# Kernel tuning notes

Hardware: AMD Instinct MI355X
Metric: run time of the kernel (lower is better)

## Reference

```python
import jax, jax.numpy as jnp
import numpy as np
from jax import lax

FILTERS = [(1, 32), (2, 32), (3, 64), (4, 128), (5, 256), (6, 512), (7, 1024)]
CHAR_VOCAB, CHAR_DIM, MAX_CHARS = 262, 16, 50
N_FILTERS = sum(n for _, n in FILTERS)  # 2048
PROJ_DIM = 512
B, S = 16, 256


def setup_inputs() -> dict:
    key = jax.random.key(0)
    ks = jax.random.split(key, 32)
    inp = {}
    inp["words"] = jax.random.randint(ks[0], (B, S), 0, 50000)
    inp["chars"] = jax.random.randint(ks[1], (B, S, MAX_CHARS), 0, CHAR_VOCAB)
    inp["char_emb"] = jax.random.normal(ks[2], (CHAR_VOCAB, CHAR_DIM), jnp.float32) * 0.1
    for i, (w, n) in enumerate(FILTERS):
        inp[f"conv_w_{i}"] = jax.random.normal(ks[3 + i], (n, CHAR_DIM, w), jnp.float32) * 0.1
        inp[f"conv_b_{i}"] = jnp.zeros((n,), jnp.float32)
    for j in range(2):
        inp[f"hw_w_{j}"] = jax.random.normal(ks[12 + j], (2 * N_FILTERS, N_FILTERS), jnp.float32) * 0.02
        # Highway init: transform bias = 0, gate bias = 1
        inp[f"hw_b_{j}"] = jnp.concatenate([jnp.zeros((N_FILTERS,), jnp.float32), jnp.ones((N_FILTERS,), jnp.float32)])
    inp["proj_w"] = jax.random.normal(ks[20], (PROJ_DIM, N_FILTERS), jnp.float32) * 0.02
    inp["proj_b"] = jnp.zeros((PROJ_DIM,), jnp.float32)
    return inp


def _char_cnn(chars, char_emb, conv_ws, conv_bs, hw_ws, hw_bs, proj_w, proj_b):
    b, s, L = chars.shape
    # (B*S, CHAR_DIM, L)
    x = char_emb[chars].reshape(b * s, L, -1).transpose(0, 2, 1)
    convs = []
    for w, bias in zip(conv_ws, conv_bs):
        # Conv1d valid, NCW layout; y: (N, num, L-width+1)
        y = lax.conv_general_dilated(x, w, (1,), "VALID", dimension_numbers=("NCH", "OIH", "NCH"))
        y = y + bias[None, :, None]
        y = jnp.max(y, axis=-1)          # max over time
        convs.append(jax.nn.relu(y))      # activation
    h = jnp.concatenate(convs, axis=-1)   # (N, 2048)
    d = h.shape[-1]
    for W, bb in zip(hw_ws, hw_bs):
        p = h @ W.T + bb
        nonlinear = jax.nn.relu(p[:, :d])
        gate = jax.nn.sigmoid(p[:, d:])
        h = gate * h + (1.0 - gate) * nonlinear
    out = h @ proj_w.T + proj_b
    return out.reshape(b, s, -1)


def reference(words, chars, char_emb,
              conv_w_0, conv_b_0, conv_w_1, conv_b_1, conv_w_2, conv_b_2,
              conv_w_3, conv_b_3, conv_w_4, conv_b_4, conv_w_5, conv_b_5,
              conv_w_6, conv_b_6, hw_w_0, hw_b_0, hw_w_1, hw_b_1, proj_w, proj_b):
    conv_ws = [conv_w_0, conv_w_1, conv_w_2, conv_w_3, conv_w_4, conv_w_5, conv_w_6]
    conv_bs = [conv_b_0, conv_b_1, conv_b_2, conv_b_3, conv_b_4, conv_b_5, conv_b_6]
    return _char_cnn(chars, char_emb, conv_ws, conv_bs, [hw_w_0, hw_w_1], [hw_b_0, hw_b_1], proj_w, proj_b)
```

## Files before the change

kernel.cpp:

```cpp
#include <hip/hip_runtime.h>
#include <hip/hip_bf16.h>


#define NTOK 4096
#define NF   2048
#define KDIM 2048
#define HID  4096
#define PDIM 512

typedef __attribute__((ext_vector_type(4))) float floatx4;
typedef __attribute__((ext_vector_type(8))) short shortx8;

__device__ inline void async_copy16(const void* g, void* l) {
  __builtin_amdgcn_global_load_lds(
      (const __attribute__((address_space(1))) void*)(uintptr_t)g,
      (__attribute__((address_space(3))) void*)(uint32_t)(uintptr_t)l,
      16, 0, 0);
}

__device__ inline void block_barrier() {
  asm volatile("" ::: "memory");
  __builtin_amdgcn_s_barrier();
  asm volatile("" ::: "memory");
}

__global__ __launch_bounds__(256) void cvt_kernel(
    const float* __restrict__ s, __hip_bfloat16* __restrict__ d, int n) {
  int i = blockIdx.x * 256 + threadIdx.x;
  if (i < n) d[i] = __float2bfloat16(s[i]);
}

__global__ __launch_bounds__(256) void cvt_hw(
    const float* __restrict__ s, __hip_bfloat16* __restrict__ d) {
  int i = blockIdx.x * 256 + threadIdx.x;
  int r = i >> 11, k = i & 2047;
  int sr = (r >> 1) + (r & 1) * 2048;
  d[i] = __float2bfloat16(s[(size_t)sr * 2048 + k]);
}

__global__ __launch_bounds__(256) void conv_wprep(
    const float* __restrict__ w0, const float* __restrict__ w1,
    const float* __restrict__ w2, const float* __restrict__ w3,
    const float* __restrict__ w4, const float* __restrict__ w5,
    const float* __restrict__ w6,
    const float* __restrict__ b0, const float* __restrict__ b1,
    const float* __restrict__ b2, const float* __restrict__ b3,
    const float* __restrict__ b4, const float* __restrict__ b5,
    const float* __restrict__ b6, const float* __restrict__ emb,
    __hip_bfloat16* __restrict__ Wb, float* __restrict__ Bc,
    __hip_bfloat16* __restrict__ embb) {
  int idx = blockIdx.x * 256 + threadIdx.x;
  const int start[7] = {0, 32, 64, 128, 256, 512, 1024};
  const float* ws[7] = {w0, w1, w2, w3, w4, w5, w6};
  const float* bs[7] = {b0, b1, b2, b3, b4, b5, b6};
  if (idx < 262144) {
    int ch = idx >> 7, kp = idx & 127;
    int f = (ch >= 32) + (ch >= 64) + (ch >= 128) + (ch >= 256) +
            (ch >= 512) + (ch >= 1024);
    int w = f + 1, lc = ch - start[f];
    int d = kp & 15, k = kp >> 4;
    float v = (k < w) ? ws[f][((size_t)lc * 16 + d) * w + k] : 0.f;
    Wb[idx] = __float2bfloat16(v);
  } else if (idx < 262144 + 2048) {
    int ch = idx - 262144;
    int f = (ch >= 32) + (ch >= 64) + (ch >= 128) + (ch >= 256) +
            (ch >= 512) + (ch >= 1024);
    Bc[ch] = bs[f][ch - start[f]];
  } else if (idx < 262144 + 2048 + 4192) {
    int e = idx - 262144 - 2048;
    embb[e] = __float2bfloat16(emb[e]);
  }
}

template <int NKT, int NT, int ROWS>
__global__ __launch_bounds__(256) void conv_k(
    const int* __restrict__ chars, const __hip_bfloat16* __restrict__ embb,
    const __hip_bfloat16* __restrict__ Wb, const float* __restrict__ bias,
    __hip_bfloat16* __restrict__ h, int chbase) {
  __shared__ __align__(16) __hip_bfloat16 Xs[2 * 4 * ROWS * 24];
  int tid = threadIdx.x, wave = tid >> 6, lane = tid & 63;
  int frow = lane & 15, q = lane >> 4;
  int chb = chbase + blockIdx.y * 64;
  int tokbase = blockIdx.x * 32;

  shortx8 wreg[NKT][4];
#pragma unroll
  for (int kt = 0; kt < NKT; ++kt)
#pragma unroll
    for (int j = 0; j < 4; ++j)
      wreg[kt][j] = *(const shortx8*)(
          Wb + (size_t)(chb + j * 16 + frow) * 128 + kt * 32 + q * 8);

  float blane = bias[chb + lane];
  int Tvj[4];
#pragma unroll
  for (int j = 0; j < 4; ++j) {
    int ch = chb + j * 16 + frow;
    int w = 1 + (ch >= 32) + (ch >= 64) + (ch >= 128) + (ch >= 256) +
            (ch >= 512) + (ch >= 1024);
    Tvj[j] = 51 - w;
  }

  auto stage = [&](int g, int buf) {
    constexpr int NST = 4 * ROWS;
#pragma unroll
    for (int rep = 0; rep < (NST + 255) / 256; ++rep) {
      int rr = tid + rep * 256;
      if (rr < NST) {
        int tk = rr / ROWS, r = rr - tk * ROWS;
        __hip_bfloat16* dst = Xs + ((size_t)(buf * 4 + tk) * ROWS + r) * 24;
        if (r < 50) {
          int c = chars[(size_t)(tokbase + g * 4 + tk) * 50 + r];
          const shortx8* e = (const shortx8*)(embb + c * 16);
          *(shortx8*)(dst) = e[0];
          *(shortx8*)(dst + 8) = e[1];
        } else if (g <= 1) {
          shortx8 z = {0, 0, 0, 0, 0, 0, 0, 0};
          *(shortx8*)(dst) = z;
          *(shortx8*)(dst + 8) = z;
        }
      }
    }
  };

  stage(0, 0);
  __syncthreads();

  const floatx4 zero = {0.f, 0.f, 0.f, 0.f};
#pragma unroll 1
  for (int g = 0; g < 8; ++g) {
    if (g < 7) stage(g + 1, (g + 1) & 1);

    const __hip_bfloat16* Xw = Xs + (size_t)((g & 1) * 4 + wave) * ROWS * 24;
    floatx4 acc[NT][4];

#pragma unroll
    for (int kt = 0; kt < NKT; ++kt) {
      int kk = kt * 2 + (q >> 1);
      int d0 = (q & 1) * 8;
      shortx8 xf[NT];
#pragma unroll
      for (int i = 0; i < NT; ++i)
        xf[i] = *(const shortx8*)(Xw + (i * 16 + frow + kk) * 24 + d0);
#pragma unroll
      for (int i = 0; i < NT; ++i)
#pragma unroll
        for (int j = 0; j < 4; ++j) {
          if (kt == 0)
            acc[i][j] = __builtin_amdgcn_mfma_f32_16x16x32_bf16(
                xf[i], wreg[0][j], zero, 0, 0, 0);
          else
            acc[i][j] = __builtin_amdgcn_mfma_f32_16x16x32_bf16(
                xf[i], wreg[kt][j], acc[i][j], 0, 0, 0);
        }
    }

    float vj[4];
#pragma unroll
    for (int j = 0; j < 4; ++j) {
      float v = -1e30f;
#pragma unroll
      for (int i = 0; i < NT; ++i) {
#pragma unroll
        for (int r = 0; r < 4; ++r) {
          if (i < 2) {
            v = fmaxf(v, acc[i][j][r]);
          } else {
            int t = i * 16 + q * 4 + r;
            if (t < Tvj[j]) v = fmaxf(v, acc[i][j][r]);
          }
        }
      }
      v = fmaxf(v, __shfl_xor(v, 16));
      v = fmaxf(v, __shfl_xor(v, 32));
      vj[j] = v;
    }
    float r0 = (q & 2) ? vj[2] : vj[0];
    float r1 = (q & 2) ? vj[3] : vj[1];
    float rv = (q & 1) ? r1 : r0;
    int tok = tokbase + g * 4 + wave;
    h[(size_t)tok * NF + chb + lane] =
        __float2bfloat16(fmaxf(rv + blane, 0.f));
    __syncthreads();
  }
}

__global__ __launch_bounds__(512, 2) void gemm_hw8(
    const __hip_bfloat16* __restrict__ A, const __hip_bfloat16* __restrict__ B,
    const float* __restrict__ hwb, __hip_bfloat16* __restrict__ Hdst) {
  __shared__ __align__(16) __hip_bfloat16 As[2 * 256 * 64];
  __shared__ __align__(16) __hip_bfloat16 Bs[2 * 256 * 64];
  int tid = threadIdx.x;
  int wave = tid >> 6, lane = tid & 63;
  int wr = wave >> 2, wc = wave & 3;
  int sr8 = lane >> 3, sc8 = lane & 7;
  int frow = lane & 15, q = lane >> 4;

  int wg = blockIdx.x;
  int swz = (wg & 7) * 32 + (wg >> 3);
  int bm = swz & 15;
  int bn = swz >> 4;

  const __hip_bfloat16* Ab = A + (size_t)bn * 256 * KDIM;
  const __hip_bfloat16* Bb = B + (size_t)bm * 256 * KDIM;

  floatx4 acc[8][4];
  const floatx4 zero = {0.f, 0.f, 0.f, 0.f};
#pragma unroll
  for (int i = 0; i < 8; ++i)
#pragma unroll
    for (int j = 0; j < 4; ++j) acc[i][j] = zero;

  auto stage_half = [&](const __hip_bfloat16* gsrc, __hip_bfloat16* lbase,
                        int d, int hf, int kb) {
#pragma unroll
    for (int it = 0; it < 2; ++it) {
      int row = hf * 128 + (wave * 2 + it) * 8;
      int r = row + sr8;
      int gc = sc8 ^ sr8;
      async_copy16(gsrc + (size_t)r * KDIM + kb + gc * 8,
                   (char*)lbase + ((size_t)d * 256 + row) * 128);
    }
  };

  shortx8 b_[4][2];
  shortx8 aA[2][2];

#define LDA(Asd, i0)                                                         \
  {                                                                          \
    _Pragma("unroll") for (int ii = 0; ii < 2; ++ii) {                       \
      _Pragma("unroll") for (int s = 0; s < 2; ++s) {                        \
        int r = wr * 128 + ((i0) + ii) * 16 + frow;                          \
        aA[ii][s] = *(const shortx8*)((Asd) + r * 64 +                       \
                                      (((s * 4 + q) ^ (frow & 7)) << 3));    \
      }                                                                      \
    }                                                                        \
  }

#define LDB(Bsd)                                                             \
  {                                                                          \
    _Pragma("unroll") for (int j = 0; j < 4; ++j) {                          \
      _Pragma("unroll") for (int s = 0; s < 2; ++s) {                        \
        int r = wc * 64 + j * 16 + frow;                                     \
        b_[j][s] = *(const shortx8*)((Bsd) + r * 64 +                        \
                                     (((s * 4 + q) ^ (frow & 7)) << 3));     \
      }                                                                      \
    }                                                                        \
  }

#define MMA2(i0)                                                             \
  {                                                                          \
    __builtin_amdgcn_s_setprio(1);                                           \
    _Pragma("unroll") for (int s = 0; s < 2; ++s) {                          \
      _Pragma("unroll") for (int ii = 0; ii < 2; ++ii) {                     \
        _Pragma("unroll") for (int j = 0; j < 4; ++j) {                      \
          acc[(i0) + ii][j] = __builtin_amdgcn_mfma_f32_16x16x32_bf16(       \
              aA[ii][s], b_[j][s], acc[(i0) + ii][j], 0, 0, 0);              \
        }                                                                    \
      }                                                                      \
    }                                                                        \
    __builtin_amdgcn_s_setprio(0);                                           \
  }

  stage_half(Bb, Bs, 0, 0, 0);
  stage_half(Bb, Bs, 0, 1, 0);
  stage_half(Ab, As, 0, 0, 0);
  stage_half(Ab, As, 0, 1, 0);
  stage_half(Bb, Bs, 1, 0, 64);
  asm volatile("s_waitcnt vmcnt(2)" ::: "memory");
  block_barrier();

  const int NTILE = KDIM / 64;
#pragma unroll 2
  for (int T = 0; T < NTILE; ++T) {
    int d = T & 1, d1 = d ^ 1;
    const __hip_bfloat16* Asd = As + d * 16384;
    const __hip_bfloat16* Bsd = Bs + d * 16384;
    int kn = (T + 1) * 64;

    LDA(Asd, 0);
    LDB(Bsd);
    if (T + 1 < NTILE) stage_half(Bb, Bs, d1, 1, kn);
    block_barrier();
    MMA2(0);
    block_barrier();

    LDA(Asd, 2);
    if (T + 1 < NTILE) stage_half(Ab, As, d1, 0, kn);
    block_barrier();
    MMA2(2);
    block_barrier();

    LDA(Asd, 4);
    if (T + 1 < NTILE) stage_half(Ab, As, d1, 1, kn);
    block_barrier();
    MMA2(4);
    block_barrier();

    LDA(Asd, 6);
    if (T + 2 < NTILE) stage_half(Bb, Bs, d, 0, kn + 64);
    block_barrier();
    MMA2(6);
    if (T + 2 < NTILE) {
      asm volatile("s_waitcnt vmcnt(2)" ::: "memory");
    } else if (T + 1 < NTILE) {
      asm volatile("s_waitcnt vmcnt(0)" ::: "memory");
    }
    block_barrier();
  }
#undef LDA
#undef LDB
#undef MMA2

  int crow0 = bn * 256 + wr * 128 + q * 4;
  int ccol0 = bm * 256 + wc * 64 + frow;
#pragma unroll
  for (int i = 0; i < 8; ++i)
#pragma unroll
    for (int j = 0; j < 4; ++j) {
      int gcol = ccol0 + j * 16;
      float bb = (gcol & 1) ? hwb[2048 + (gcol >> 1)] : hwb[gcol >> 1];
#pragma unroll
      for (int r = 0; r < 4; ++r) {
        int row = crow0 + i * 16 + r;
        float v = acc[i][j][r] + bb;
        float partner = __shfl_xor(v, 1);
        if (!(lane & 1)) {
          float gte = 1.f / (1.f + expf(-partner));
          int ch = gcol >> 1;
          float hold = __bfloat162float(A[(size_t)row * 2048 + ch]);
          float hnew = gte * hold + (1.f - gte) * fmaxf(v, 0.f);
          Hdst[(size_t)row * 2048 + ch] = __float2bfloat16(hnew);
        }
      }
    }
}

__global__ __launch_bounds__(256) void gemm_proj(
    const __hip_bfloat16* __restrict__ A, const __hip_bfloat16* __restrict__ B,
    float* __restrict__ C, const float* __restrict__ bias) {
  const int K = KDIM;
  __shared__ __align__(16) __hip_bfloat16 As[32 * 64];
  __shared__ __align__(16) __hip_bfloat16 Bs[128 * 64];
  int tid = threadIdx.x;
  int wave = tid >> 6, lane = tid & 63;
  int wr = wave >> 1, wc = wave & 1;
  int bn = blockIdx.y, bm = blockIdx.x;

  int sr8 = lane >> 3, sc8 = lane & 7;
  int frow = lane & 15, q = lane >> 4;

  floatx4 acc[4];
  floatx4 zero = {0.f, 0.f, 0.f, 0.f};
#pragma unroll
  for (int j = 0; j < 4; ++j) acc[j] = zero;

  const __hip_bfloat16* Ab = A + (size_t)bn * 32 * K;
  const __hip_bfloat16* Bb = B + (size_t)bm * 128 * K;

  for (int kb = 0; kb < K; kb += 64) {
    __syncthreads();
    {
      int r = wave * 8 + sr8;
      int gc = sc8 ^ (r & 7);
      async_copy16(Ab + (size_t)r * K + kb + gc * 8, (char*)As + wave * 1024);
    }
#pragma unroll
    for (int it = 0; it < 4; ++it) {
      int seg = wave * 4 + it;
      int r = seg * 8 + sr8;
      int gc = sc8 ^ (r & 7);
      async_copy16(Bb + (size_t)r * K + kb + gc * 8, (char*)Bs + seg * 1024);
    }
    __syncthreads();

#pragma unroll
    for (int s = 0; s < 2; ++s) {
      shortx8 af, bf[4];
      {
        int r = wr * 16 + frow;
        af = *(const shortx8*)(As + r * 64 + ((s * 4 + q) ^ (r & 7)) * 8);
      }
#pragma unroll
      for (int j = 0; j < 4; ++j) {
        int r = wc * 64 + j * 16 + frow;
        bf[j] = *(const shortx8*)(Bs + r * 64 + ((s * 4 + q) ^ (r & 7)) * 8);
      }
#pragma unroll
      for (int j = 0; j < 4; ++j)
        acc[j] = __builtin_amdgcn_mfma_f32_16x16x32_bf16(af, bf[j], acc[j],
                                                          0, 0, 0);
    }
  }

  int crow0 = bn * 32 + wr * 16 + q * 4;
  int ccol0 = bm * 128 + wc * 64 + frow;
#pragma unroll
  for (int j = 0; j < 4; ++j) {
    int c = ccol0 + j * 16;
#pragma unroll
    for (int r = 0; r < 4; ++r) {
      int row = crow0 + r;
      C[(size_t)row * PDIM + c] = acc[j][r] + bias[c];
    }
  }
}

extern "C" void kernel_launch(void* const* d_in, const int* in_sizes, int n_in,
                              void* d_out, int out_size, void* d_ws, size_t ws_size,
                              hipStream_t stream) {
  const int*   chars  = (const int*)d_in[1];
  const float* emb    = (const float*)d_in[2];
  const float* cw[7];
  const float* cb[7];
  for (int i = 0; i < 7; ++i) {
    cw[i] = (const float*)d_in[3 + 2 * i];
    cb[i] = (const float*)d_in[4 + 2 * i];
  }
  const float* hw_w0  = (const float*)d_in[17];
  const float* hw_b0  = (const float*)d_in[18];
  const float* hw_w1  = (const float*)d_in[19];
  const float* hw_b1  = (const float*)d_in[20];
  const float* proj_w = (const float*)d_in[21];
  const float* proj_b = (const float*)d_in[22];
  float* out = (float*)d_out;

  char* ws = (char*)d_ws;
  __hip_bfloat16* h      = (__hip_bfloat16*)(ws);
  __hip_bfloat16* h2     = (__hip_bfloat16*)(ws + (16ull << 20));
  __hip_bfloat16* convWb = (__hip_bfloat16*)(ws + (32ull << 20));
  float*          convBc = (float*)(ws + (32ull << 20) + 524288);
  __hip_bfloat16* embb   = (__hip_bfloat16*)(ws + (32ull << 20) + 524288 + 8192);
  __hip_bfloat16* w0b    = (__hip_bfloat16*)(ws + (48ull << 20));
  __hip_bfloat16* w1b    = (__hip_bfloat16*)(ws + (64ull << 20));
  __hip_bfloat16* pwb    = (__hip_bfloat16*)(ws + (80ull << 20));

  cvt_hw<<<(HID * KDIM) / 256, 256, 0, stream>>>(hw_w0, w0b);
  cvt_hw<<<(HID * KDIM) / 256, 256, 0, stream>>>(hw_w1, w1b);
  cvt_kernel<<<(PDIM * KDIM) / 256, 256, 0, stream>>>(proj_w, pwb, PDIM * KDIM);
  conv_wprep<<<(262144 + 2048 + 4192 + 255) / 256, 256, 0, stream>>>(
      cw[0], cw[1], cw[2], cw[3], cw[4], cw[5], cw[6],
      cb[0], cb[1], cb[2], cb[3], cb[4], cb[5], cb[6], emb,
      convWb, convBc, embb);

  conv_k<1, 4, 72><<<dim3(128, 1), 256, 0, stream>>>(chars, embb, convWb,
                                                     convBc, h, 0);
  conv_k<2, 3, 56><<<dim3(128, 3), 256, 0, stream>>>(chars, embb, convWb,
                                                     convBc, h, 64);
  conv_k<3, 3, 56><<<dim3(128, 12), 256, 0, stream>>>(chars, embb, convWb,
                                                      convBc, h, 256);
  conv_k<4, 3, 56><<<dim3(128, 16), 256, 0, stream>>>(chars, embb, convWb,
                                                      convBc, h, 1024);

  gemm_hw8<<<dim3(256), 512, 0, stream>>>(h, w0b, hw_b0, h2);
  gemm_hw8<<<dim3(256), 512, 0, stream>>>(h2, w1b, hw_b1, h);
  gemm_proj<<<dim3(PDIM / 128, NTOK / 32), 256, 0, stream>>>(h, pwb, out,
                                                             proj_b);
}
```

Baseline: 469.3 us.

## Vectorize weight conversions and restructure highway GEMM main loop with fewer barriers

```diff
diff --git a/kernel.cpp b/kernel.cpp
--- a/kernel.cpp
+++ b/kernel.cpp
@@ -24,18 +24,36 @@
   asm volatile("" ::: "memory");
 }
 
-__global__ __launch_bounds__(256) void cvt_kernel(
-    const float* __restrict__ s, __hip_bfloat16* __restrict__ d, int n) {
+__global__ __launch_bounds__(256) void cvt8_kernel(
+    const float* __restrict__ s, __hip_bfloat16* __restrict__ d, int n8) {
   int i = blockIdx.x * 256 + threadIdx.x;
-  if (i < n) d[i] = __float2bfloat16(s[i]);
-}
-
-__global__ __launch_bounds__(256) void cvt_hw(
+  if (i < n8) {
+    floatx4 v0 = *(const floatx4*)(s + (size_t)i * 8);
+    floatx4 v1 = *(const floatx4*)(s + (size_t)i * 8 + 4);
+    union { shortx8 v; __hip_bfloat16 h[8]; } u;
+#pragma unroll
+    for (int t = 0; t < 4; ++t) u.h[t] = __float2bfloat16(v0[t]);
+#pragma unroll
+    for (int t = 0; t < 4; ++t) u.h[4 + t] = __float2bfloat16(v1[t]);
+    *(shortx8*)(d + (size_t)i * 8) = u.v;
+  }
+}
+
+__global__ __launch_bounds__(256) void cvt_hw8(
     const float* __restrict__ s, __hip_bfloat16* __restrict__ d) {
   int i = blockIdx.x * 256 + threadIdx.x;
-  int r = i >> 11, k = i & 2047;
+  int r = i >> 8;
+  int kb = (i & 255) * 8;
   int sr = (r >> 1) + (r & 1) * 2048;
-  d[i] = __float2bfloat16(s[(size_t)sr * 2048 + k]);
+  const float* src = s + (size_t)sr * 2048 + kb;
+  floatx4 v0 = *(const floatx4*)(src);
+  floatx4 v1 = *(const floatx4*)(src + 4);
+  union { shortx8 v; __hip_bfloat16 h[8]; } u;
+#pragma unroll
+  for (int t = 0; t < 4; ++t) u.h[t] = __float2bfloat16(v0[t]);
+#pragma unroll
+  for (int t = 0; t < 4; ++t) u.h[4 + t] = __float2bfloat16(v1[t]);
+  *(shortx8*)(d + (size_t)r * 2048 + kb) = u.v;
 }
 
 __global__ __launch_bounds__(256) void conv_wprep(
@@ -223,51 +241,40 @@
     }
   };
 
-  shortx8 b_[4][2];
-  shortx8 aA[2][2];
-
-#define LDA(Asd, i0)                                                         \
-  {                                                                          \
-    _Pragma("unroll") for (int ii = 0; ii < 2; ++ii) {                       \
-      _Pragma("unroll") for (int s = 0; s < 2; ++s) {                        \
-        int r = wr * 128 + ((i0) + ii) * 16 + frow;                          \
-        aA[ii][s] = *(const shortx8*)((Asd) + r * 64 +                       \
-                                      (((s * 4 + q) ^ (frow & 7)) << 3));    \
-      }                                                                      \
-    }                                                                        \
-  }
-
-#define LDB(Bsd)                                                             \
-  {                                                                          \
-    _Pragma("unroll") for (int j = 0; j < 4; ++j) {                          \
-      _Pragma("unroll") for (int s = 0; s < 2; ++s) {                        \
-        int r = wc * 64 + j * 16 + frow;                                     \
-        b_[j][s] = *(const shortx8*)((Bsd) + r * 64 +                        \
-                                     (((s * 4 + q) ^ (frow & 7)) << 3));     \
-      }                                                                      \
-    }                                                                        \
-  }
-
-#define MMA2(i0)                                                             \
-  {                                                                          \
-    __builtin_amdgcn_s_setprio(1);                                           \
-    _Pragma("unroll") for (int s = 0; s < 2; ++s) {                          \
-      _Pragma("unroll") for (int ii = 0; ii < 2; ++ii) {                     \
-        _Pragma("unroll") for (int j = 0; j < 4; ++j) {                      \
-          acc[(i0) + ii][j] = __builtin_amdgcn_mfma_f32_16x16x32_bf16(       \
-              aA[ii][s], b_[j][s], acc[(i0) + ii][j], 0, 0, 0);              \
-        }                                                                    \
-      }                                                                      \
-    }                                                                        \
-    __builtin_amdgcn_s_setprio(0);                                           \
-  }
-
+  auto lda2 = [&](shortx8* dst2, const __hip_bfloat16* Asd, int i0, int s) {
+#pragma unroll
+    for (int ii = 0; ii < 2; ++ii) {
+      int r = wr * 128 + (i0 + ii) * 16 + frow;
+      dst2[ii] = *(const shortx8*)(Asd + r * 64 +
+                                   (((s * 4 + q) ^ (frow & 7)) << 3));
+    }
+  };
+  auto ldb4 = [&](shortx8* dst4, const __hip_bfloat16* Bsd, int s) {
+#pragma unroll
+    for (int j = 0; j < 4; ++j) {
+      int r = wc * 64 + j * 16 + frow;
+      dst4[j] = *(const shortx8*)(Bsd + r * 64 +
+                                  (((s * 4 + q) ^ (frow & 7)) << 3));
+    }
+  };
+  auto mma8 = [&](const shortx8* aX, const shortx8* bX, int i0) {
+    __builtin_amdgcn_s_setprio(1);
+#pragma unroll
+    for (int ii = 0; ii < 2; ++ii)
+#pragma unroll
+      for (int j = 0; j < 4; ++j)
+        acc[i0 + ii][j] = __builtin_amdgcn_mfma_f32_16x16x32_bf16(
+            aX[ii], bX[j], acc[i0 + ii][j], 0, 0, 0);
+    __builtin_amdgcn_s_setprio(0);
+  };
+
+  stage_half(Ab, As, 0, 0, 0);
+  stage_half(Ab, As, 0, 1, 0);
   stage_half(Bb, Bs, 0, 0, 0);
   stage_half(Bb, Bs, 0, 1, 0);
-  stage_half(Ab, As, 0, 0, 0);
-  stage_half(Ab, As, 0, 1, 0);
   stage_half(Bb, Bs, 1, 0, 64);
-  asm volatile("s_waitcnt vmcnt(2)" ::: "memory");
+  stage_half(Bb, Bs, 1, 1, 64);
+  asm volatile("s_waitcnt vmcnt(4)" ::: "memory");
   block_barrier();
 
   const int NTILE = KDIM / 64;
@@ -278,39 +285,39 @@
     const __hip_bfloat16* Bsd = Bs + d * 16384;
     int kn = (T + 1) * 64;
 
-    LDA(Asd, 0);
-    LDB(Bsd);
-    if (T + 1 < NTILE) stage_half(Bb, Bs, d1, 1, kn);
+    shortx8 aU[2], aV[2], b0[4], b1[4];
+    ldb4(b0, Bsd, 0);
+    lda2(aU, Asd, 0, 0);
+    if (T + 1 < NTILE) {
+      stage_half(Ab, As, d1, 0, kn);
+      stage_half(Ab, As, d1, 1, kn);
+    }
+    lda2(aV, Asd, 2, 0);
+    mma8(aU, b0, 0);
+    lda2(aU, Asd, 4, 0);
+    mma8(aV, b0, 2);
+    lda2(aV, Asd, 6, 0);
+    ldb4(b1, Bsd, 1);
+    mma8(aU, b0, 4);
+    lda2(aU, Asd, 0, 1);
+    mma8(aV, b0, 6);
+    lda2(aV, Asd, 2, 1);
+    mma8(aU, b1, 0);
     block_barrier();
-    MMA2(0);
-    block_barrier();
-
-    LDA(Asd, 2);
-    if (T + 1 < NTILE) stage_half(Ab, As, d1, 0, kn);
-    block_barrier();
-    MMA2(2);
-    block_barrier();
-
-    LDA(Asd, 4);
-    if (T + 1 < NTILE) stage_half(Ab, As, d1, 1, kn);
-    block_barrier();
-    MMA2(4);
-    block_barrier();
-
-    LDA(Asd, 6);
     if (T + 2 < NTILE) stage_half(Bb, Bs, d, 0, kn + 64);
-    block_barrier();
-    MMA2(6);
+    lda2(aU, Asd, 4, 1);
+    mma8(aV, b1, 2);
+    if (T + 2 < NTILE) stage_half(Bb, Bs, d, 1, kn + 64);
+    lda2(aV, Asd, 6, 1);
+    mma8(aU, b1, 4);
+    mma8(aV, b1, 6);
     if (T + 2 < NTILE) {
-      asm volatile("s_waitcnt vmcnt(2)" ::: "memory");
+      asm volatile("s_waitcnt vmcnt(4)" ::: "memory");
     } else if (T + 1 < NTILE) {
       asm volatile("s_waitcnt vmcnt(0)" ::: "memory");
     }
     block_barrier();
   }
-#undef LDA
-#undef LDB
-#undef MMA2
 
   int crow0 = bn * 256 + wr * 128 + q * 4;
   int ccol0 = bm * 256 + wc * 64 + frow;
@@ -435,9 +442,10 @@
   __hip_bfloat16* w1b    = (__hip_bfloat16*)(ws + (64ull << 20));
   __hip_bfloat16* pwb    = (__hip_bfloat16*)(ws + (80ull << 20));
 
-  cvt_hw<<<(HID * KDIM) / 256, 256, 0, stream>>>(hw_w0, w0b);
-  cvt_hw<<<(HID * KDIM) / 256, 256, 0, stream>>>(hw_w1, w1b);
-  cvt_kernel<<<(PDIM * KDIM) / 256, 256, 0, stream>>>(proj_w, pwb, PDIM * KDIM);
+  cvt_hw8<<<(HID * KDIM / 8) / 256, 256, 0, stream>>>(hw_w0, w0b);
+  cvt_hw8<<<(HID * KDIM / 8) / 256, 256, 0, stream>>>(hw_w1, w1b);
+  cvt8_kernel<<<(PDIM * KDIM / 8) / 256, 256, 0, stream>>>(proj_w, pwb,
+                                                           PDIM * KDIM / 8);
   conv_wprep<<<(262144 + 2048 + 4192 + 255) / 256, 256, 0, stream>>>(
       cw[0], cw[1], cw[2], cw[3], cw[4], cw[5], cw[6],
       cb[0], cb[1], cb[2], cb[3], cb[4], cb[5], cb[6], emb,
```

Result: faster. 448.4 us (-4.4%).
